# Optimization experiments

Hardware: AMD Instinct MI355X
Metric: run time of the kernel (lower is better)

## Reference

```python
import jax, jax.numpy as jnp
import numpy as np

N, E, NB, P = 100000, 1600000, 1000, 500000


def gcn_conv(x, edge_index, W, b):
    # PyG GCNConv: add self-loops, symmetric D^-1/2 (A+I) D^-1/2 normalization,
    # linear transform, bias.
    n = x.shape[0]
    loop = jnp.arange(n, dtype=edge_index.dtype)
    src = jnp.concatenate([edge_index[0], loop])
    dst = jnp.concatenate([edge_index[1], loop])
    deg = jax.ops.segment_sum(jnp.ones(src.shape[0], x.dtype), dst, num_segments=n)
    dinv = jnp.where(deg > 0, jax.lax.rsqrt(deg), 0.0)
    norm = dinv[src] * dinv[dst]                       # [E+n]
    xw = x @ W                                          # [n, out]
    out = jax.ops.segment_sum(xw[src] * norm[:, None], dst, num_segments=n)
    return out + b


def setup_inputs() -> dict:
    key = jax.random.key(0)
    ks = jax.random.split(key, 12)
    x = jax.random.normal(ks[0], (N, 27), jnp.float32)
    edge_index = jax.random.randint(ks[1], (2, E), 0, N, dtype=jnp.int32)
    bank = jax.random.normal(ks[2], (NB, 27), jnp.float32)
    node1 = jax.random.randint(ks[3], (P,), 0, N + NB, dtype=jnp.int32)
    node2 = jax.random.randint(ks[4], (P,), 0, N + NB, dtype=jnp.int32)

    def lin(k, fan_in, fan_out):
        s = 1.0 / np.sqrt(fan_in)
        kw, kb = jax.random.split(k)
        W = jax.random.uniform(kw, (fan_in, fan_out), jnp.float32, -s, s)
        b = jax.random.uniform(kb, (fan_out,), jnp.float32, -s, s)
        return W, b

    W1, b1 = lin(ks[5], 27, 60)
    W2, b2 = lin(ks[6], 60, 50)
    Wb, bb = lin(ks[7], 27, 50)
    Wf1, bf1 = lin(ks[8], 100, 40)
    Wf2, bf2 = lin(ks[9], 40, 20)
    Wf3, bf3 = lin(ks[10], 20, 4)
    return dict(x=x, bank=bank, W1=W1, b1=b1, W2=W2, b2=b2, Wb=Wb, bb=bb,
                Wf1=Wf1, bf1=bf1, Wf2=Wf2, bf2=bf2, Wf3=Wf3, bf3=bf3,
                edge_index=edge_index, node1=node1, node2=node2)


def reference(x, bank, W1, b1, W2, b2, Wb, bb, Wf1, bf1, Wf2, bf2, Wf3, bf3,
              edge_index, node1, node2):
    h = gcn_conv(x, edge_index, W1, b1)                 # [N, 60]
    h = gcn_conv(h, edge_index, W2, b2)                 # [N, 50]
    bk = bank @ Wb + bb                                 # [NB, 50]
    allh = jnp.concatenate([h, bk], axis=0)             # [N+NB, 50]
    z = jnp.concatenate([allh[node1], allh[node2]], axis=1)  # [P, 100]
    z = z @ Wf1 + bf1
    z = z @ Wf2 + bf2
    z = z @ Wf3 + bf3                                   # [P, 4]
    return jax.nn.softmax(z, axis=0)                    # softmax over dim 0, as in source
```

## Files before the change

kernel.cpp:

```cpp
#include <hip/hip_runtime.h>
#include <math.h>

#define N_NODES 100000
#define N_EDGES 1600000
#define NB_BANK 1000
#define N_PAIRS 500000

#define BUCK_SHIFT 8
#define BUCK_NODES 256
#define NBUCK 391
#define BCAP 5504
#define EPB 4096
#define NSCAT 391
#define NZB4 489
#define SMASK 0x1FFFF
#define ECACHE 11

struct Consts {
  float C[27*8];
  float Rb[27*8];
  float u[8];
  float vg[8];
  float vb[8];
};

__device__ void precompute_body(
    const float* __restrict__ W1, const float* __restrict__ b1,
    const float* __restrict__ W2, const float* __restrict__ b2,
    const float* __restrict__ Wb, const float* __restrict__ bb,
    const float* __restrict__ Wf1, const float* __restrict__ bf1,
    const float* __restrict__ Wf2, const float* __restrict__ bf2,
    const float* __restrict__ Wf3, const float* __restrict__ bf3,
    Consts* __restrict__ cst) {
  __shared__ float A[40*4];
  __shared__ float T[100*4];
  __shared__ float B[60*8];
  __shared__ float cvec[4];
  const int tid = threadIdx.x;
  const int nt = blockDim.x;

  for (int idx = tid; idx < 160; idx += nt) {
    int r = idx >> 2, k = idx & 3;
    float s = 0.f;
    for (int j = 0; j < 20; ++j) s += Wf2[r*20+j] * Wf3[j*4+k];
    A[idx] = s;
  }
  __syncthreads();
  for (int idx = tid; idx < 400; idx += nt) {
    int r = idx >> 2, k = idx & 3;
    float s = 0.f;
    for (int j = 0; j < 40; ++j) s += Wf1[r*40+j] * A[j*4+k];
    T[idx] = s;
  }
  if (tid < 4) {
    float s = bf3[tid];
    for (int j = 0; j < 40; ++j) s += bf1[j] * A[j*4+tid];
    for (int j = 0; j < 20; ++j) s += bf2[j] * Wf3[j*4+tid];
    cvec[tid] = s;
  }
  __syncthreads();
  for (int idx = tid; idx < 480; idx += nt) {
    int r = idx >> 3, k = idx & 7;
    int half = k >> 2, kk = k & 3;
    float s = 0.f;
    for (int j = 0; j < 50; ++j) s += W2[r*50+j] * T[(half*50+j)*4+kk];
    B[idx] = s;
  }
  __syncthreads();
  for (int idx = tid; idx < 456; idx += nt) {
    if (idx < 216) {
      int r = idx >> 3, k = idx & 7;
      float s = 0.f;
      for (int j = 0; j < 60; ++j) s += W1[r*60+j] * B[j*8+k];
      cst->C[idx] = s;
    } else if (idx < 432) {
      int i2 = idx - 216;
      int r = i2 >> 3, k = i2 & 7, half = k >> 2, kk = k & 3;
      float s = 0.f;
      for (int j = 0; j < 50; ++j) s += Wb[r*50+j] * T[(half*50+j)*4+kk];
      cst->Rb[i2] = s;
    } else if (idx < 440) {
      int k = idx - 432;
      float s = 0.f;
      for (int j = 0; j < 60; ++j) s += b1[j] * B[j*8+k];
      cst->u[k] = s;
    } else if (idx < 448) {
      int k = idx - 440, half = k >> 2, kk = k & 3;
      float s = (half == 0) ? cvec[kk] : 0.f;
      for (int j = 0; j < 50; ++j) s += b2[j] * T[(half*50+j)*4+kk];
      cst->vg[k] = s;
    } else {
      int k = idx - 448, half = k >> 2, kk = k & 3;
      float s = (half == 0) ? cvec[kk] : 0.f;
      for (int j = 0; j < 50; ++j) s += bb[j] * T[(half*50+j)*4+kk];
      cst->vb[k] = s;
    }
  }
}

__global__ __launch_bounds__(1024) void k_scatter(
    const int* __restrict__ ei, int* __restrict__ bcnt, int* __restrict__ ebuf,
    const float* __restrict__ W1, const float* __restrict__ b1,
    const float* __restrict__ W2, const float* __restrict__ b2,
    const float* __restrict__ Wb, const float* __restrict__ bb,
    const float* __restrict__ Wf1, const float* __restrict__ bf1,
    const float* __restrict__ Wf2, const float* __restrict__ bf2,
    const float* __restrict__ Wf3, const float* __restrict__ bf3,
    Consts* __restrict__ cst) {
  if (blockIdx.x == NSCAT) {
    precompute_body(W1, b1, W2, b2, Wb, bb, Wf1, bf1, Wf2, bf2, Wf3, bf3, cst);
    return;
  }
  __shared__ int hist[NBUCK];
  __shared__ int base[NBUCK];
  const int t = threadIdx.x;
  const int e0 = blockIdx.x * EPB;
  int dcache[EPB / 1024];
  int scache[EPB / 1024];
  if (t < NBUCK) hist[t] = 0;
  __syncthreads();
#pragma unroll
  for (int i = 0; i < EPB / 1024; ++i) {
    int e = e0 + i * 1024 + t;
    int d = -1, s = 0;
    if (e < N_EDGES) { d = ei[N_EDGES + e]; s = ei[e]; }
    dcache[i] = d;
    scache[i] = s;
    if (d >= 0) atomicAdd(&hist[d >> BUCK_SHIFT], 1);
  }
  __syncthreads();
  if (t < NBUCK) {
    int h = hist[t];
    base[t] = h ? (t * BCAP + atomicAdd(&bcnt[t], h)) : 0;
    hist[t] = 0;
  }
  __syncthreads();
#pragma unroll
  for (int i = 0; i < EPB / 1024; ++i) {
    int d = dcache[i];
    if (d >= 0) {
      int b = d >> BUCK_SHIFT;
      int pos = base[b] + atomicAdd(&hist[b], 1);
      ebuf[pos] = ((d & (BUCK_NODES - 1)) << 17) | scache[i];
    }
  }
}

__global__ __launch_bounds__(512) void k_degfill_x8(
    const int* __restrict__ bcnt, const int* __restrict__ ebuf,
    const float* __restrict__ x, const Consts* __restrict__ cst,
    float* __restrict__ dinv, int* __restrict__ rbeg, int* __restrict__ rend,
    int* __restrict__ csr, float* __restrict__ Xs) {
  __shared__ int cnt[BUCK_NODES];
  __shared__ int lcur[BUCK_NODES];
  __shared__ float sdinv[BUCK_NODES];
  __shared__ float xs[BUCK_NODES * 27];
  const int b = blockIdx.x;
  const int t = threadIdx.x;
  int ecache[ECACHE];
  if (t < BUCK_NODES) cnt[t] = 0;
  __syncthreads();
  const int beg = b * BCAP, end = beg + bcnt[b];
  int ne = 0;
  for (int j = beg + t; j < end; j += 512, ++ne) {
    int code = ebuf[j];
    ecache[ne] = code;
    atomicAdd(&cnt[code >> 17], 1);
  }
  const int xbase = b * (BUCK_NODES * 27);
  for (int j = t; j < BUCK_NODES * 27; j += 512) {
    int g = xbase + j;
    xs[j] = (g < N_NODES * 27) ? x[g] : 0.f;
  }
  __syncthreads();
  int v = (t < BUCK_NODES) ? cnt[t] : 0;
  for (int off = 1; off < BUCK_NODES; off <<= 1) {
    int u = (t < BUCK_NODES && t >= off) ? cnt[t - off] : 0;
    __syncthreads();
    if (t < BUCK_NODES) cnt[t] += u;
    __syncthreads();
  }
  if (t < BUCK_NODES) {
    const int node = (b << BUCK_SHIFT) + t;
    const int excl = beg + cnt[t] - v;
    lcur[t] = excl;
    float dv = rsqrtf((float)v + 1.0f);
    sdinv[t] = dv;
    if (node < N_NODES) {
      rbeg[node] = excl;
      rend[node] = excl + v;
      dinv[node] = dv;
    }
  }
  __syncthreads();
  for (int i = 0; i < ne; ++i) {
    int code = ecache[i];
    int pos = atomicAdd(&lcur[code >> 17], 1);
    csr[pos] = code & SMASK;
  }
  for (int idx = t; idx < BUCK_NODES * 8; idx += 512) {
    int li = idx >> 3, k = idx & 7;
    int node = (b << BUCK_SHIFT) + li;
    if (node < N_NODES) {
      float s = 0.f;
      for (int c = 0; c < 27; ++c) s += xs[li*27+c] * cst->C[c*8+k];
      Xs[(size_t)node*8+k] = s * sdinv[li];
    }
  }
}

__global__ __launch_bounds__(256) void k_gather1(const int* __restrict__ rbeg,
                                                 const int* __restrict__ rend,
                                                 const int* __restrict__ csr,
                                                 const float* __restrict__ dinv,
                                                 const float2* __restrict__ Xs2,
                                                 float2* __restrict__ Ys2,
                                                 float* __restrict__ dvec) {
  int t = blockIdx.x * 256 + threadIdx.x;
  int d = t >> 2, q = t & 3;
  if (d >= N_NODES) return;
  const int beg = rbeg[d], end = rend[d];
  const float nd = dinv[d];
  float2 self = Xs2[d*4 + q];
  float ax = self.x, ay = self.y;
  float dsum = nd;
  int j = beg;
  if (j + 8 <= end) {
    int s0 = csr[j],   s1 = csr[j+1], s2 = csr[j+2], s3 = csr[j+3];
    int s4 = csr[j+4], s5 = csr[j+5], s6 = csr[j+6], s7 = csr[j+7];
    for (;;) {
      float2 a0 = Xs2[s0*4+q], a1 = Xs2[s1*4+q], a2 = Xs2[s2*4+q], a3 = Xs2[s3*4+q];
      float2 a4 = Xs2[s4*4+q], a5 = Xs2[s5*4+q], a6 = Xs2[s6*4+q], a7 = Xs2[s7*4+q];
      float d0 = 0.f, d1 = 0.f, d2 = 0.f, d3 = 0.f;
      float d4 = 0.f, d5 = 0.f, d6 = 0.f, d7 = 0.f;
      if (q == 0) {
        d0 = dinv[s0]; d1 = dinv[s1]; d2 = dinv[s2]; d3 = dinv[s3];
        d4 = dinv[s4]; d5 = dinv[s5]; d6 = dinv[s6]; d7 = dinv[s7];
      }
      int jn = j + 8;
      bool more = (jn + 8 <= end);
      int u0, u1, u2, u3, u4, u5, u6, u7;
      if (more) {
        u0 = csr[jn];   u1 = csr[jn+1]; u2 = csr[jn+2]; u3 = csr[jn+3];
        u4 = csr[jn+4]; u5 = csr[jn+5]; u6 = csr[jn+6]; u7 = csr[jn+7];
      } else {
        u0 = u1 = u2 = u3 = u4 = u5 = u6 = u7 = 0;
      }
      ax += ((a0.x + a1.x) + (a2.x + a3.x)) + ((a4.x + a5.x) + (a6.x + a7.x));
      ay += ((a0.y + a1.y) + (a2.y + a3.y)) + ((a4.y + a5.y) + (a6.y + a7.y));
      if (q == 0)
        dsum += ((d0 + d1) + (d2 + d3)) + ((d4 + d5) + (d6 + d7));
      j = jn;
      if (!more) break;
      s0 = u0; s1 = u1; s2 = u2; s3 = u3;
      s4 = u4; s5 = u5; s6 = u6; s7 = u7;
    }
  }
  if (j + 4 <= end) {
    int a = csr[j], b = csr[j+1], c = csr[j+2], e = csr[j+3];
    float2 p0 = Xs2[a*4+q], p1 = Xs2[b*4+q], p2 = Xs2[c*4+q], p3 = Xs2[e*4+q];
    ax += (p0.x + p1.x) + (p2.x + p3.x);
    ay += (p0.y + p1.y) + (p2.y + p3.y);
    if (q == 0) dsum += (dinv[a] + dinv[b]) + (dinv[c] + dinv[e]);
    j += 4;
  }
  for (; j < end; ++j) {
    int s = csr[j];
    float2 a = Xs2[s*4+q];
    ax += a.x; ay += a.y;
    if (q == 0) dsum += dinv[s];
  }
  float nn = nd * nd;
  Ys2[t] = make_float2(nn * ax, nn * ay);
  if (q == 0) dvec[d] = nd * dsum;
}

__global__ __launch_bounds__(256) void k_gather2g(const int* __restrict__ rbeg,
                                                  const int* __restrict__ rend,
                                                  const int* __restrict__ csr,
                                                  const float* __restrict__ dinv,
                                                  const float2* __restrict__ Ys2,
                                                  const float* __restrict__ dvec,
                                                  const float* __restrict__ bank,
                                                  const Consts* __restrict__ cst,
                                                  float2* __restrict__ gall2) {
  int t = blockIdx.x * 256 + threadIdx.x;
  int d = t >> 2, q = t & 3;
  if (d >= N_NODES + NB_BANK) return;
  int c0 = 2*q, c1 = 2*q + 1;
  if (d >= N_NODES) {
    int bk = d - N_NODES;
    float sx = cst->vb[c0], sy = cst->vb[c1];
    for (int cc = 0; cc < 27; ++cc) {
      float bv = bank[bk*27+cc];
      sx += bv * cst->Rb[cc*8+c0];
      sy += bv * cst->Rb[cc*8+c1];
    }
    gall2[t] = make_float2(sx, sy);
    return;
  }
  const int beg = rbeg[d], end = rend[d];
  float2 self = Ys2[d*4 + q];
  float ax = self.x, ay = self.y;
  int j = beg;
  if (j + 8 <= end) {
    int s0 = csr[j],   s1 = csr[j+1], s2 = csr[j+2], s3 = csr[j+3];
    int s4 = csr[j+4], s5 = csr[j+5], s6 = csr[j+6], s7 = csr[j+7];
    for (;;) {
      float2 a0 = Ys2[s0*4+q], a1 = Ys2[s1*4+q], a2 = Ys2[s2*4+q], a3 = Ys2[s3*4+q];
      float2 a4 = Ys2[s4*4+q], a5 = Ys2[s5*4+q], a6 = Ys2[s6*4+q], a7 = Ys2[s7*4+q];
      int jn = j + 8;
      bool more = (jn + 8 <= end);
      int u0, u1, u2, u3, u4, u5, u6, u7;
      if (more) {
        u0 = csr[jn];   u1 = csr[jn+1]; u2 = csr[jn+2]; u3 = csr[jn+3];
        u4 = csr[jn+4]; u5 = csr[jn+5]; u6 = csr[jn+6]; u7 = csr[jn+7];
      } else {
        u0 = u1 = u2 = u3 = u4 = u5 = u6 = u7 = 0;
      }
      ax += ((a0.x + a1.x) + (a2.x + a3.x)) + ((a4.x + a5.x) + (a6.x + a7.x));
      ay += ((a0.y + a1.y) + (a2.y + a3.y)) + ((a4.y + a5.y) + (a6.y + a7.y));
      j = jn;
      if (!more) break;
      s0 = u0; s1 = u1; s2 = u2; s3 = u3;
      s4 = u4; s5 = u5; s6 = u6; s7 = u7;
    }
  }
  if (j + 4 <= end) {
    int a = csr[j], b = csr[j+1], c = csr[j+2], e = csr[j+3];
    float2 p0 = Ys2[a*4+q], p1 = Ys2[b*4+q], p2 = Ys2[c*4+q], p3 = Ys2[e*4+q];
    ax += (p0.x + p1.x) + (p2.x + p3.x);
    ay += (p0.y + p1.y) + (p2.y + p3.y);
    j += 4;
  }
  for (; j < end; ++j) {
    float2 a = Ys2[csr[j]*4+q];
    ax += a.x; ay += a.y;
  }
  float nd = dinv[d], dv = dvec[d];
  gall2[t] = make_float2(nd * ax + dv * cst->u[c0] + cst->vg[c0],
                         nd * ay + dv * cst->u[c1] + cst->vg[c1]);
}

__device__ inline void sm_merge(float4& m1, float4& s1,
                                const float4 m2, const float4 s2) {
  float4 M;
  M.x = fmaxf(m1.x, m2.x); M.y = fmaxf(m1.y, m2.y);
  M.z = fmaxf(m1.z, m2.z); M.w = fmaxf(m1.w, m2.w);
  s1.x = s1.x * expf(m1.x - M.x) + s2.x * expf(m2.x - M.x);
  s1.y = s1.y * expf(m1.y - M.y) + s2.y * expf(m2.y - M.y);
  s1.z = s1.z * expf(m1.z - M.z) + s2.z * expf(m2.z - M.z);
  s1.w = s1.w * expf(m1.w - M.w) + s2.w * expf(m2.w - M.w);
  m1 = M;
}

__global__ __launch_bounds__(256) void k_z(const int* __restrict__ node1,
                                           const int* __restrict__ node2,
                                           const float* __restrict__ gall,
                                           float4* __restrict__ bs_m,
                                           float4* __restrict__ bs_s) {
  const int S = NZB4 * 256;
  int p0 = blockIdx.x * 256 + threadIdx.x;
  float4 m = make_float4(-1e30f, -1e30f, -1e30f, -1e30f);
  float4 s = make_float4(0.f, 0.f, 0.f, 0.f);
#pragma unroll
  for (int i = 0; i < 4; ++i) {
    int p = p0 + i * S;
    if (p < N_PAIRS) {
      int n1 = node1[p], n2 = node2[p];
      const float4 a = *(const float4*)(gall + (size_t)n1*8);
      const float4 b = *(const float4*)(gall + (size_t)n2*8 + 4);
      float4 zv = make_float4(a.x+b.x, a.y+b.y, a.z+b.z, a.w+b.w);
      sm_merge(m, s, zv, make_float4(1.f, 1.f, 1.f, 1.f));
    }
  }
  __shared__ float4 lm[256], ls[256];
  lm[threadIdx.x] = m; ls[threadIdx.x] = s;
  __syncthreads();
  for (int st = 128; st > 0; st >>= 1) {
    if (threadIdx.x < st) {
      float4 mm = lm[threadIdx.x], ss = ls[threadIdx.x];
      sm_merge(mm, ss, lm[threadIdx.x + st], ls[threadIdx.x + st]);
      lm[threadIdx.x] = mm; ls[threadIdx.x] = ss;
    }
    __syncthreads();
  }
  if (threadIdx.x == 0) { bs_m[blockIdx.x] = lm[0]; bs_s[blockIdx.x] = ls[0]; }
}

__global__ __launch_bounds__(256) void k_final(const int* __restrict__ node1,
                                               const int* __restrict__ node2,
                                               const float* __restrict__ gall,
                                               const float4* __restrict__ bs_m,
                                               const float4* __restrict__ bs_s,
                                               float* __restrict__ out) {
  float4 m = make_float4(-1e30f, -1e30f, -1e30f, -1e30f);
  float4 s = make_float4(0.f, 0.f, 0.f, 0.f);
  for (int i = threadIdx.x; i < NZB4; i += 256)
    sm_merge(m, s, bs_m[i], bs_s[i]);
  __shared__ float4 lm[256], ls[256];
  lm[threadIdx.x] = m; ls[threadIdx.x] = s;
  __syncthreads();
  for (int st = 128; st > 0; st >>= 1) {
    if (threadIdx.x < st) {
      float4 mm = lm[threadIdx.x], ss = ls[threadIdx.x];
      sm_merge(mm, ss, lm[threadIdx.x + st], ls[threadIdx.x + st]);
      lm[threadIdx.x] = mm; ls[threadIdx.x] = ss;
    }
    __syncthreads();
  }
  const float4 M = lm[0], S4 = ls[0];
  const float i0 = 1.f / S4.x, i1 = 1.f / S4.y;
  const float i2 = 1.f / S4.z, i3 = 1.f / S4.w;
  const int S = NZB4 * 256;
  int p0 = blockIdx.x * 256 + threadIdx.x;
#pragma unroll
  for (int i = 0; i < 4; ++i) {
    int p = p0 + i * S;
    if (p < N_PAIRS) {
      int n1 = node1[p], n2 = node2[p];
      const float4 a = *(const float4*)(gall + (size_t)n1*8);
      const float4 b = *(const float4*)(gall + (size_t)n2*8 + 4);
      float4 zv = make_float4(a.x+b.x, a.y+b.y, a.z+b.z, a.w+b.w);
      float4 o = make_float4(expf(zv.x - M.x) * i0, expf(zv.y - M.y) * i1,
                             expf(zv.z - M.z) * i2, expf(zv.w - M.w) * i3);
      ((float4*)out)[p] = o;
    }
  }
}

extern "C" void kernel_launch(void* const* d_in, const int* in_sizes, int n_in,
                              void* d_out, int out_size, void* d_ws, size_t ws_size,
                              hipStream_t stream) {
  const float* x    = (const float*)d_in[0];
  const float* bank = (const float*)d_in[1];
  const float* W1   = (const float*)d_in[2];
  const float* b1   = (const float*)d_in[3];
  const float* W2   = (const float*)d_in[4];
  const float* b2   = (const float*)d_in[5];
  const float* Wb   = (const float*)d_in[6];
  const float* bb   = (const float*)d_in[7];
  const float* Wf1  = (const float*)d_in[8];
  const float* bf1  = (const float*)d_in[9];
  const float* Wf2  = (const float*)d_in[10];
  const float* bf2  = (const float*)d_in[11];
  const float* Wf3  = (const float*)d_in[12];
  const float* bf3  = (const float*)d_in[13];
  const int* ei     = (const int*)d_in[14];
  const int* node1  = (const int*)d_in[15];
  const int* node2  = (const int*)d_in[16];
  float* out = (float*)d_out;

  char* w = (char*)d_ws;
  size_t off = 0;
  auto take = [&](size_t bytes) -> char* {
    char* p = w + off;
    off = (off + bytes + 255) & ~(size_t)255;
    return p;
  };
  Consts* cst    = (Consts*)take(sizeof(Consts));
  int*    bcnt   = (int*)take(NBUCK * 4);
  float*  dinv   = (float*)take(N_NODES * 4);
  int*    rbeg   = (int*)take(N_NODES * 4);
  int*    rend   = (int*)take(N_NODES * 4);
  int*    csr    = (int*)take((size_t)NBUCK * BCAP * 4);
  float*  Xs     = (float*)take((size_t)N_NODES * 8 * 4);
  float*  Ys     = (float*)take((size_t)N_NODES * 8 * 4);
  float*  dvec   = (float*)take(N_NODES * 4);
  float*  gall   = (float*)take((size_t)(N_NODES + NB_BANK) * 8 * 4);
  int*    ebuf   = (int*)take((size_t)NBUCK * BCAP * 4);
  float4* bs_m   = (float4*)take((size_t)NZB4 * 16);
  float4* bs_s   = (float4*)take((size_t)NZB4 * 16);

  hipMemsetAsync(bcnt, 0, NBUCK * 4, stream);

  k_scatter<<<NSCAT + 1, 1024, 0, stream>>>(ei, bcnt, ebuf, W1, b1, W2, b2,
                                            Wb, bb, Wf1, bf1, Wf2, bf2,
                                            Wf3, bf3, cst);
  k_degfill_x8<<<NBUCK, 512, 0, stream>>>(bcnt, ebuf, x, cst,
                                          dinv, rbeg, rend, csr, Xs);
  k_gather1<<<(N_NODES * 4 + 255) / 256, 256, 0, stream>>>(
      rbeg, rend, csr, dinv, (const float2*)Xs, (float2*)Ys, dvec);
  k_gather2g<<<((N_NODES + NB_BANK) * 4 + 255) / 256, 256, 0, stream>>>(
      rbeg, rend, csr, dinv, (const float2*)Ys, dvec, bank, cst, (float2*)gall);
  k_z<<<NZB4, 256, 0, stream>>>(node1, node2, gall, bs_m, bs_s);
  k_final<<<NZB4, 256, 0, stream>>>(node1, node2, gall, bs_m, bs_s, out);
}
```

Measured before the change: 200.8 us.

## Sort nodes by degree within buckets to balance gather wavefront work

In the degree/fill kernel, the nodes of each 256-node bucket are counting-sorted by in-degree (capped at 63) into a permutation array. Both gather kernels then walk nodes in that permuted order, so lanes of a wavefront handle nodes with similar edge counts and diverge less in their loop trip counts. The cost is an extra permutation load per thread, scattered output writes instead of contiguous ones, and a few extra block syncs plus a serial prefix scan in the fill kernel.

```diff
diff --git a/kernel.cpp b/kernel.cpp
--- a/kernel.cpp
+++ b/kernel.cpp
@@ -9,6 +9,7 @@
 #define BUCK_SHIFT 8
 #define BUCK_NODES 256
 #define NBUCK 391
+#define NSLOT (NBUCK * BUCK_NODES)
 #define BCAP 5504
 #define EPB 4096
 #define NSCAT 391
@@ -150,7 +151,7 @@
     const int* __restrict__ bcnt, const int* __restrict__ ebuf,
     const float* __restrict__ x, const Consts* __restrict__ cst,
     float* __restrict__ dinv, int* __restrict__ rbeg, int* __restrict__ rend,
-    int* __restrict__ csr, float* __restrict__ Xs) {
+    int* __restrict__ csr, float* __restrict__ Xs, int* __restrict__ perm) {
   __shared__ int cnt[BUCK_NODES];
   __shared__ int lcur[BUCK_NODES];
   __shared__ float sdinv[BUCK_NODES];
@@ -198,6 +199,25 @@
     int pos = atomicAdd(&lcur[code >> 17], 1);
     csr[pos] = code & SMASK;
   }
+  __syncthreads();
+  if (t < 64) lcur[t] = 0;
+  __syncthreads();
+  int cls = 0, lrank = 0;
+  if (t < BUCK_NODES) {
+    cls = v < 63 ? v : 63;
+    lrank = atomicAdd(&lcur[cls], 1);
+  }
+  __syncthreads();
+  if (t == 0) {
+    int run = 0;
+    for (int i = 0; i < 64; ++i) { int c = lcur[i]; lcur[i] = run; run += c; }
+  }
+  __syncthreads();
+  if (t < BUCK_NODES) {
+    int node = (b << BUCK_SHIFT) + t;
+    int pos = lcur[cls] + lrank;
+    perm[(b << BUCK_SHIFT) + pos] = (node < N_NODES) ? node : N_NODES;
+  }
   for (int idx = t; idx < BUCK_NODES * 8; idx += 512) {
     int li = idx >> 3, k = idx & 7;
     int node = (b << BUCK_SHIFT) + li;
@@ -209,7 +229,8 @@
   }
 }
 
-__global__ __launch_bounds__(256) void k_gather1(const int* __restrict__ rbeg,
+__global__ __launch_bounds__(256) void k_gather1(const int* __restrict__ perm,
+                                                 const int* __restrict__ rbeg,
                                                  const int* __restrict__ rend,
                                                  const int* __restrict__ csr,
                                                  const float* __restrict__ dinv,
@@ -217,7 +238,9 @@
                                                  float2* __restrict__ Ys2,
                                                  float* __restrict__ dvec) {
   int t = blockIdx.x * 256 + threadIdx.x;
-  int d = t >> 2, q = t & 3;
+  int slot = t >> 2, q = t & 3;
+  if (slot >= NSLOT) return;
+  int d = perm[slot];
   if (d >= N_NODES) return;
   const int beg = rbeg[d], end = rend[d];
   const float nd = dinv[d];
@@ -271,11 +294,12 @@
     if (q == 0) dsum += dinv[s];
   }
   float nn = nd * nd;
-  Ys2[t] = make_float2(nn * ax, nn * ay);
+  Ys2[d*4 + q] = make_float2(nn * ax, nn * ay);
   if (q == 0) dvec[d] = nd * dsum;
 }
 
-__global__ __launch_bounds__(256) void k_gather2g(const int* __restrict__ rbeg,
+__global__ __launch_bounds__(256) void k_gather2g(const int* __restrict__ perm,
+                                                  const int* __restrict__ rbeg,
                                                   const int* __restrict__ rend,
                                                   const int* __restrict__ csr,
                                                   const float* __restrict__ dinv,
@@ -285,20 +309,22 @@
                                                   const Consts* __restrict__ cst,
                                                   float2* __restrict__ gall2) {
   int t = blockIdx.x * 256 + threadIdx.x;
-  int d = t >> 2, q = t & 3;
-  if (d >= N_NODES + NB_BANK) return;
+  int slot = t >> 2, q = t & 3;
+  if (slot >= NSLOT + NB_BANK) return;
   int c0 = 2*q, c1 = 2*q + 1;
-  if (d >= N_NODES) {
-    int bk = d - N_NODES;
+  if (slot >= NSLOT) {
+    int bk = slot - NSLOT;
     float sx = cst->vb[c0], sy = cst->vb[c1];
     for (int cc = 0; cc < 27; ++cc) {
       float bv = bank[bk*27+cc];
       sx += bv * cst->Rb[cc*8+c0];
       sy += bv * cst->Rb[cc*8+c1];
     }
-    gall2[t] = make_float2(sx, sy);
+    gall2[((size_t)(N_NODES + bk))*4 + q] = make_float2(sx, sy);
     return;
   }
+  int d = perm[slot];
+  if (d >= N_NODES) return;
   const int beg = rbeg[d], end = rend[d];
   float2 self = Ys2[d*4 + q];
   float ax = self.x, ay = self.y;
@@ -338,8 +364,8 @@
     ax += a.x; ay += a.y;
   }
   float nd = dinv[d], dv = dvec[d];
-  gall2[t] = make_float2(nd * ax + dv * cst->u[c0] + cst->vg[c0],
-                         nd * ay + dv * cst->u[c1] + cst->vg[c1]);
+  gall2[d*4 + q] = make_float2(nd * ax + dv * cst->u[c0] + cst->vg[c0],
+                               nd * ay + dv * cst->u[c1] + cst->vg[c1]);
 }
 
 __device__ inline void sm_merge(float4& m1, float4& s1,
@@ -469,6 +495,7 @@
   float*  dvec   = (float*)take(N_NODES * 4);
   float*  gall   = (float*)take((size_t)(N_NODES + NB_BANK) * 8 * 4);
   int*    ebuf   = (int*)take((size_t)NBUCK * BCAP * 4);
+  int*    perm   = (int*)take((size_t)NSLOT * 4);
   float4* bs_m   = (float4*)take((size_t)NZB4 * 16);
   float4* bs_s   = (float4*)take((size_t)NZB4 * 16);
 
@@ -478,11 +505,12 @@
                                             Wb, bb, Wf1, bf1, Wf2, bf2,
                                             Wf3, bf3, cst);
   k_degfill_x8<<<NBUCK, 512, 0, stream>>>(bcnt, ebuf, x, cst,
-                                          dinv, rbeg, rend, csr, Xs);
-  k_gather1<<<(N_NODES * 4 + 255) / 256, 256, 0, stream>>>(
-      rbeg, rend, csr, dinv, (const float2*)Xs, (float2*)Ys, dvec);
-  k_gather2g<<<((N_NODES + NB_BANK) * 4 + 255) / 256, 256, 0, stream>>>(
-      rbeg, rend, csr, dinv, (const float2*)Ys, dvec, bank, cst, (float2*)gall);
+                                          dinv, rbeg, rend, csr, Xs, perm);
+  k_gather1<<<(NSLOT * 4 + 255) / 256, 256, 0, stream>>>(
+      perm, rbeg, rend, csr, dinv, (const float2*)Xs, (float2*)Ys, dvec);
+  k_gather2g<<<((NSLOT + NB_BANK) * 4 + 255) / 256, 256, 0, stream>>>(
+      perm, rbeg, rend, csr, dinv, (const float2*)Ys, dvec, bank, cst,
+      (float2*)gall);
   k_z<<<NZB4, 256, 0, stream>>>(node1, node2, gall, bs_m, bs_s);
   k_final<<<NZB4, 256, 0, stream>>>(node1, node2, gall, bs_m, bs_s, out);
 }
```

After: 214.8 us. 7.0% more time.
